# Kernel tuning notes

Measured on AMD Instinct MI355X. Metric: run time of the kernel, lower is better.

## Reference

```python
import jax, jax.numpy as jnp
import numpy as np

N_HEAD = 8
D_IN = 64
D_EMB = 128
B, S = 8, 2048
TEMP = D_EMB ** 0.5
EPS = 1e-6
NEG = -1e30


def setup_inputs() -> dict:
    key = jax.random.key(0)
    ks = jax.random.split(key, 10)
    Q = jax.random.normal(ks[0], (B, S, D_IN), jnp.float32)
    K = jax.random.normal(ks[1], (B, S, D_IN), jnp.float32)
    V = jax.random.normal(ks[2], (B, S, D_IN), jnp.float32)
    QMask = jax.random.randint(ks[3], (B, 1, 1, S), 0, 2).astype(jnp.float32)
    s_in = 1.0 / np.sqrt(D_IN)
    s_emb = 1.0 / np.sqrt(D_EMB)
    s_cat = 1.0 / np.sqrt(N_HEAD * D_EMB)
    W_in = jax.random.uniform(ks[4], (D_EMB, D_IN), jnp.float32, -s_in, s_in)
    W_mh = jax.random.uniform(ks[5], (N_HEAD * D_EMB, D_EMB), jnp.float32, -s_emb, s_emb)
    W_fc = jax.random.uniform(ks[6], (D_EMB, N_HEAD * D_EMB), jnp.float32, -s_cat, s_cat)
    ln_g = jnp.ones((D_EMB,), jnp.float32)
    ln_b = jnp.zeros((D_EMB,), jnp.float32)
    return {"Q": Q, "K": K, "V": V, "QMask": QMask,
            "W_in": W_in, "W_mh": W_mh, "W_fc": W_fc,
            "ln_g": ln_g, "ln_b": ln_b}


def reference(Q, K, V, QMask, W_in, W_mh, W_fc, ln_g, ln_b):
    b, ql = Q.shape[0], Q.shape[1]
    kl = K.shape[1]
    # shared input embedding
    Qe = jnp.einsum('bsi,ei->bse', Q, W_in)  # [B,Sq,D_EMB]
    Ke = jnp.einsum('bsi,ei->bse', K, W_in)
    Ve = jnp.einsum('bsi,ei->bse', V, W_in)
    residual = Qe
    # multi-head projection -> [B,S,H,D] -> [B,H,S,D]
    q = jnp.einsum('bse,fe->bsf', Qe, W_mh).reshape(b, ql, N_HEAD, D_EMB).transpose(0, 2, 1, 3)
    k = jnp.einsum('bse,fe->bsf', Ke, W_mh).reshape(b, kl, N_HEAD, D_EMB).transpose(0, 2, 1, 3)
    v = jnp.einsum('bse,fe->bsf', Ve, W_mh).reshape(b, kl, N_HEAD, D_EMB).transpose(0, 2, 1, 3)
    attn = jnp.einsum('bhqd,bhkd->bhqk', q / TEMP, k)
    attn = attn + (1.0 - QMask) * NEG
    attn = jax.nn.softmax(attn, axis=-1)
    out = jnp.einsum('bhqk,bhkd->bhqd', attn, v)  # [B,H,Sq,D]
    # faithful to original: view without transposing heads back
    out = out.reshape(b, ql, N_HEAD * D_EMB)
    out = jnp.einsum('bsf,ef->bse', out, W_fc) + residual
    mu = jnp.mean(out, axis=-1, keepdims=True)
    var = jnp.var(out, axis=-1, keepdims=True)
    out = (out - mu) / jnp.sqrt(var + EPS) * ln_g + ln_b
    return out
```

## Files before the change

### kernel.cpp

```cpp
#include <hip/hip_runtime.h>
#include <hip/hip_bf16.h>
#include <cstdint>

typedef __attribute__((ext_vector_type(8))) short short8;
typedef __attribute__((ext_vector_type(4))) float f32x4;
typedef __attribute__((ext_vector_type(16))) float f32x16;
typedef unsigned short u16;
typedef unsigned int u32;

__device__ __forceinline__ u16 f2bf(float f) {
    union { float f; u32 u; } v; v.f = f;
    u32 u = v.u;
    u = (u + 0x7fffu + ((u >> 16) & 1u)) >> 16;
    return (u16)u;
}

__device__ __forceinline__ float fexp2(float x) {
    float r;
    asm("v_exp_f32 %0, %1" : "=v"(r) : "v"(x));
    return r;
}

__device__ __forceinline__ u32 pk_bf16(float lo, float hi) {
    u32 r;
    asm("v_cvt_pk_bf16_f32 %0, %1, %2" : "=v"(r) : "v"(lo), "v"(hi));
    return r;
}

__device__ __forceinline__ void pl32swap(u32& a, u32& b) {
#if __has_builtin(__builtin_amdgcn_permlane32_swap)
    auto r = __builtin_amdgcn_permlane32_swap((int)a, (int)b, false, false);
    a = (u32)r[0]; b = (u32)r[1];
#else
    u32 ax = (u32)__shfl_xor((int)a, 32), bx = (u32)__shfl_xor((int)b, 32);
    bool hi = (threadIdx.x & 32) != 0;
    u32 na = hi ? bx : a;
    u32 nb = hi ? b : ax;
    a = na; b = nb;
#endif
}

__device__ __forceinline__ void gload_lds16(const u16* g, u16* l) {
    __builtin_amdgcn_global_load_lds((const __attribute__((address_space(1))) void*)g,
                                     (__attribute__((address_space(3))) void*)l, 16, 0, 0);
}

__device__ __forceinline__ short8 make_pa(float p0, float p1, float p2, float p3,
                                          float p4, float p5, float p6, float p7) {
    u32 a1 = pk_bf16(p0, p1), b1 = pk_bf16(p4, p5);
    u32 a2 = pk_bf16(p2, p3), b2 = pk_bf16(p6, p7);
    pl32swap(a1, b1); pl32swap(a2, b2);
    union { u32 w[4]; short8 s; } u;
    u.w[0] = a1; u.w[1] = a2; u.w[2] = b1; u.w[3] = b2;
    return u.s;
}

__global__ void prep_kernel(const float* __restrict__ W_in,
                            const float* __restrict__ W_mh,
                            const float* __restrict__ W_fc,
                            const float* __restrict__ qmask,
                            u16* __restrict__ wcomb, u16* __restrict__ wfc16,
                            u16* __restrict__ win16,
                            u16* __restrict__ pos, int* __restrict__ cnt) {
    if (blockIdx.x >= 800) {
        if (threadIdx.x >= 64) return;
        int b = blockIdx.x - 800, t = threadIdx.x;
        int base = b * 2048 + t * 32;
        int c = 0;
#pragma unroll
        for (int i = 0; i < 32; ++i) c += (qmask[base + i] != 0.0f) ? 1 : 0;
        int inc = c;
#pragma unroll
        for (int dd = 1; dd < 64; dd <<= 1) {
            int v = __shfl_up(inc, dd);
            if (t >= dd) inc += v;
        }
        int run = inc - c;
#pragma unroll
        for (int i = 0; i < 32; ++i) {
            bool mk = (qmask[base + i] != 0.0f);
            pos[base + i] = mk ? (u16)run : (u16)0xFFFF;
            run += mk ? 1 : 0;
        }
        if (t == 63) cnt[b] = inc;
        return;
    }
    int idx = blockIdx.x * 256 + threadIdx.x;
    if (idx < 1024 * 64) {
        int f = idx >> 6, i = idx & 63;
        float acc = 0.f;
        for (int e = 0; e < 128; ++e)
            acc += W_mh[f * 128 + e] * W_in[e * 64 + i];
        wcomb[idx] = f2bf(acc);
    }
    int idx2 = idx - 65536;
    if (idx2 >= 0 && idx2 < 128 * 1024)
        wfc16[idx2] = f2bf(W_fc[idx2]);
    int idx3 = idx - 65536 - 131072;
    if (idx3 >= 0 && idx3 < 128 * 64)
        win16[idx3] = f2bf(W_in[idx3]);
}

__global__ __launch_bounds__(256) void qkv_kernel(
    const float* __restrict__ K, const float* __restrict__ V,
    const u16* __restrict__ wcomb, const u16* __restrict__ pos,
    u16* __restrict__ kb, u16* __restrict__ vrow) {
    __shared__ __align__(16) u16 ot[64 * 264];
    int w = threadIdx.x >> 6, lane = threadIdx.x & 63;
    int g = lane >> 4, c15 = lane & 15;
    const float* X = blockIdx.z == 0 ? K : V;

    int Rrow = blockIdx.x * 64 + w * 16 + c15;
    short8 af[2];
#pragma unroll
    for (int c = 0; c < 2; ++c) {
        const float* p = X + (size_t)Rrow * 64 + 8 * g + 32 * c;
        float4 fa = *(const float4*)(p);
        float4 fb = *(const float4*)(p + 4);
        short8 a;
        a[0] = (short)f2bf(fa.x); a[1] = (short)f2bf(fa.y);
        a[2] = (short)f2bf(fa.z); a[3] = (short)f2bf(fa.w);
        a[4] = (short)f2bf(fb.x); a[5] = (short)f2bf(fb.y);
        a[6] = (short)f2bf(fb.z); a[7] = (short)f2bf(fb.w);
        af[c] = a;
    }
    int colbase = blockIdx.y * 256;
    f32x4 acc[16];
#pragma unroll
    for (int i = 0; i < 16; ++i) acc[i] = {0.f, 0.f, 0.f, 0.f};
#pragma unroll
    for (int cb = 0; cb < 16; ++cb) {
        int col = colbase + cb * 16 + c15;
#pragma unroll
        for (int c = 0; c < 2; ++c) {
            short8 bfr = *(const short8*)(wcomb + (size_t)col * 64 + 8 * g + 32 * c);
            acc[cb] = __builtin_amdgcn_mfma_f32_16x16x32_bf16(af[c], bfr, acc[cb], 0, 0, 0);
        }
    }
    int r0 = w * 16 + 4 * g;
#pragma unroll
    for (int cb = 0; cb < 16; ++cb)
#pragma unroll
        for (int r = 0; r < 4; ++r)
            ot[(r0 + r) * 264 + cb * 16 + c15] = f2bf(acc[cb][r]);
    __syncthreads();
    u16* dstbuf = blockIdx.z == 0 ? kb : vrow;
#pragma unroll
    for (int it = 0; it < 8; ++it) {
        int chunk = threadIdx.x + it * 256;
        int row = chunk >> 5, cc = chunk & 31;
        int R = blockIdx.x * 64 + row;
        u16 p = pos[R];
        if (p != 0xFFFF) {
            int b = R >> 11;
            int col0 = colbase + cc * 8;
            int h = col0 >> 7, d = col0 & 127;
            *(uint4*)(dstbuf + ((size_t)(b * 8 + h) * 2048 + p) * 128 + d) =
                *(const uint4*)(ot + row * 264 + cc * 8);
        }
    }
}

__global__ __launch_bounds__(256) void vtrans_kernel(
    const u16* __restrict__ vrow, const int* __restrict__ cnt,
    u16* __restrict__ vT) {
    int t = blockIdx.x, bh = blockIdx.y, b = bh >> 3;
    int L = cnt[b];
    if (t * 64 >= L) return;
    __shared__ __align__(16) u32 tl[128 * 32];
    const u16* src = vrow + ((size_t)bh * 2048 + t * 64) * 128;
#pragma unroll
    for (int task = 0; task < 2; ++task) {
        int id = threadIdx.x + task * 256;
        int i = id >> 4, c = id & 15;
        int r0 = 2 * i, r1 = 2 * i + 1;
        uint4 A = {0, 0, 0, 0}, Bv = {0, 0, 0, 0};
        if (t * 64 + r0 < L) A  = *(const uint4*)(src + (size_t)r0 * 128 + c * 8);
        if (t * 64 + r1 < L) Bv = *(const uint4*)(src + (size_t)r1 * 128 + c * 8);
        const u32* aw = (const u32*)&A;
        const u32* bw = (const u32*)&Bv;
#pragma unroll
        for (int j = 0; j < 4; ++j) {
            u32 lo  = (aw[j] & 0xFFFFu) | (bw[j] << 16);
            u32 hi2 = (aw[j] >> 16) | (bw[j] & 0xFFFF0000u);
            int d0 = 8 * c + 2 * j, d1 = d0 + 1;
            int h0 = ((d0 & 7) ^ ((d0 >> 3) & 7)) << 2;
            int h1 = ((d1 & 7) ^ ((d1 >> 3) & 7)) << 2;
            tl[d0 * 32 + (i ^ h0)] = lo;
            tl[d1 * 32 + (i ^ h1)] = hi2;
        }
    }
    __syncthreads();
    int d = threadIdx.x >> 1, half = threadIdx.x & 1;
    int hd = (d & 7) ^ ((d >> 3) & 7);
#pragma unroll
    for (int jc = 0; jc < 4; ++jc) {
        int chunk = (half * 4 + jc) ^ hd;
        int kcg = t * 8 + half * 4 + jc;
        *(uint4*)(vT + (((size_t)bh * 256 + kcg) * 128 + d) * 8) =
            *(const uint4*)(&tl[d * 32 + chunk * 4]);
    }
}

__global__ __launch_bounds__(512, 2) void attn_kernel(
    const float* __restrict__ Qin, const u16* __restrict__ wcomb,
    const u16* __restrict__ kbuf, const u16* __restrict__ vTc,
    const int* __restrict__ cnt,
    const u16* __restrict__ wfc16, const u16* __restrict__ win16,
    const float* __restrict__ ln_g, const float* __restrict__ ln_b,
    float* __restrict__ out) {
    __shared__ __align__(16) u16 smem[32768];
    __shared__ float2 pls[32][4];

    const int w = threadIdx.x >> 6, lane = threadIdx.x & 63;
    const int hi = lane >> 5, l31 = lane & 31;
    const int g = lane >> 4, c15 = lane & 15;
    const int bh = blockIdx.x, qt = blockIdx.y;
    const int b = bh >> 3, h = bh & 7;
    const int L = cnt[b];
    const int nt = (L + 63) >> 6;

    const u16* kbbh = kbuf + (size_t)bh * 2048 * 128;
    const u16* vTbh = vTc + (size_t)bh * 262144;

    u16* ktb0 = smem;
    u16* vtb0 = smem + 16384;

    auto stage = [&](int buf, int tt) {
#pragma unroll
        for (int c = 0; c < 2; ++c) {
            int rl = (c * 8 + w) * 4 + (lane >> 4);
            int ck = (lane & 15) ^ (rl & 7);
            gload_lds16(kbbh + ((size_t)(tt * 64 + rl)) * 128 + ck * 8,
                        ktb0 + buf * 8192 + (c * 8 + w) * 512);
            int ci = c * 512 + w * 64 + lane;
            gload_lds16(vTbh + ((size_t)tt * 1024 + ci) * 8,
                        vtb0 + buf * 8192 + (c * 512 + w * 64) * 8);
        }
    };

    stage(0, 0);

    const float invT2 = 0.12751743f;
    const int q0 = qt * 256 + w * 32;
    const float* qrow = Qin + ((size_t)b * 2048 + q0 + l31) * 64;
    short8 bq[4];
#pragma unroll
    for (int s = 0; s < 4; ++s) {
        const float* p = qrow + s * 16 + hi * 8;
        float4 fa = *(const float4*)(p);
        float4 fb = *(const float4*)(p + 4);
        short8 a;
        a[0] = (short)f2bf(fa.x); a[1] = (short)f2bf(fa.y);
        a[2] = (short)f2bf(fa.z); a[3] = (short)f2bf(fa.w);
        a[4] = (short)f2bf(fb.x); a[5] = (short)f2bf(fb.y);
        a[6] = (short)f2bf(fb.z); a[7] = (short)f2bf(fb.w);
        bq[s] = a;
    }
    short8 qf[8];
#pragma unroll
    for (int dblk = 0; dblk < 4; ++dblk) {
        f32x16 c2;
#pragma unroll
        for (int r = 0; r < 16; ++r) c2[r] = 0.f;
        const u16* wrow = wcomb + (size_t)(h * 128 + dblk * 32 + l31) * 64 + hi * 8;
#pragma unroll
        for (int s = 0; s < 4; ++s) {
            short8 wa = *(const short8*)(wrow + s * 16);
            c2 = __builtin_amdgcn_mfma_f32_32x32x16_bf16(wa, bq[s], c2, 0, 0, 0);
        }
        qf[2 * dblk] = make_pa(c2[0] * invT2, c2[1] * invT2, c2[2] * invT2, c2[3] * invT2,
                               c2[4] * invT2, c2[5] * invT2, c2[6] * invT2, c2[7] * invT2);
        qf[2 * dblk + 1] = make_pa(c2[8] * invT2, c2[9] * invT2, c2[10] * invT2, c2[11] * invT2,
                                   c2[12] * invT2, c2[13] * invT2, c2[14] * invT2, c2[15] * invT2);
    }

    f32x16 o[4];
#pragma unroll
    for (int i = 0; i < 4; ++i)
#pragma unroll
        for (int r = 0; r < 16; ++r) o[i][r] = 0.f;
    float m = -1e30f, lsum = 0.f;

    int cur = 0;
    __syncthreads();

    for (int t = 0; t < nt; ++t) {
        if (t + 1 < nt) stage(cur ^ 1, t + 1);
        const u16* ktb = ktb0 + cur * 8192;
        const u16* vtb = vtb0 + cur * 8192;

        f32x16 st0, st1;
#pragma unroll
        for (int r = 0; r < 16; ++r) { st0[r] = 0.f; st1[r] = 0.f; }
        int k0 = l31, k1 = 32 + l31;
#pragma unroll
        for (int ds = 0; ds < 8; ++ds) {
            int sw = ((ds * 2 + hi) ^ (l31 & 7)) << 3;
            short8 kf0 = *(const short8*)(ktb + (k0 << 7) + sw);
            short8 kf1 = *(const short8*)(ktb + (k1 << 7) + sw);
            st0 = __builtin_amdgcn_mfma_f32_32x32x16_bf16(kf0, qf[ds], st0, 0, 0, 0);
            st1 = __builtin_amdgcn_mfma_f32_32x32x16_bf16(kf1, qf[ds], st1, 0, 0, 0);
        }
        if (t == nt - 1) {
#pragma unroll
            for (int r = 0; r < 16; ++r) {
                int kl = (r & 3) + 8 * (r >> 2) + 4 * hi;
                st0[r] = (t * 64 + kl < L) ? st0[r] : -1e30f;
                st1[r] = (t * 64 + 32 + kl < L) ? st1[r] : -1e30f;
            }
        }
        float mx = st0[0];
#pragma unroll
        for (int r = 1; r < 16; ++r) mx = fmaxf(mx, st0[r]);
#pragma unroll
        for (int r = 0; r < 16; ++r) mx = fmaxf(mx, st1[r]);
        mx = fmaxf(mx, __shfl_xor(mx, 32));
        if (__any(mx - m > 11.0f)) {
            float mn = fmaxf(m, mx);
            float corr = fexp2(m - mn);
            m = mn;
            lsum *= corr;
#pragma unroll
            for (int r = 0; r < 16; ++r) {
                float cc = __shfl(corr, (r & 3) + 8 * (r >> 2) + 4 * hi);
                o[0][r] *= cc; o[1][r] *= cc; o[2][r] *= cc; o[3][r] *= cc;
            }
        }
        float p0a[16], p1a[16];
#pragma unroll
        for (int r = 0; r < 16; ++r) { p0a[r] = fexp2(st0[r] - m); p1a[r] = fexp2(st1[r] - m); }
        float s0 = 0.f, s1 = 0.f, s2 = 0.f, s3 = 0.f;
#pragma unroll
        for (int r = 0; r < 16; r += 4) {
            s0 += p0a[r]; s1 += p0a[r + 1]; s2 += p0a[r + 2]; s3 += p0a[r + 3];
            s0 += p1a[r]; s1 += p1a[r + 1]; s2 += p1a[r + 2]; s3 += p1a[r + 3];
        }
        float tot = (s0 + s1) + (s2 + s3);
        tot += __shfl_xor(tot, 32);
        lsum += tot;
        short8 pa0 = make_pa(p0a[0], p0a[1], p0a[2], p0a[3], p0a[4], p0a[5], p0a[6], p0a[7]);
        short8 pa1 = make_pa(p0a[8], p0a[9], p0a[10], p0a[11], p0a[12], p0a[13], p0a[14], p0a[15]);
        short8 pa2 = make_pa(p1a[0], p1a[1], p1a[2], p1a[3], p1a[4], p1a[5], p1a[6], p1a[7]);
        short8 pa3 = make_pa(p1a[8], p1a[9], p1a[10], p1a[11], p1a[12], p1a[13], p1a[14], p1a[15]);
#pragma unroll
        for (int dblk = 0; dblk < 4; ++dblk) {
#pragma unroll
            for (int ks = 0; ks < 4; ++ks) {
                short8 vf = *(const short8*)(vtb +
                    ((((ks * 2 + hi) << 7) + (dblk << 5) + l31) << 3));
                short8 pa = (ks == 0) ? pa0 : (ks == 1) ? pa1 : (ks == 2) ? pa2 : pa3;
                o[dblk] = __builtin_amdgcn_mfma_f32_32x32x16_bf16(pa, vf, o[dblk], 0, 0, 0);
            }
        }
        __syncthreads();
        cur ^= 1;
    }

    u16* epi = smem;
    float invl = 1.0f / lsum;
#pragma unroll
    for (int r = 0; r < 16; ++r) {
        int kl = (r & 3) + 8 * (r >> 2) + 4 * hi;
        float iv = __shfl(invl, kl);
        int row_local = w * 4 + (kl >> 3);
        int cb2 = (kl & 7) * 16 + (l31 >> 3);
#pragma unroll
        for (int dblk = 0; dblk < 4; ++dblk) {
            int cw = cb2 + dblk * 4;
            epi[(cw * 32 + row_local) * 8 + (l31 & 7)] = f2bf(o[dblk][r] * iv);
        }
    }
    __syncthreads();

    const int rg = w >> 2, cg = w & 3;
    const int srow0 = h * 256 + qt * 32;
    const int row16 = rg * 16 + c15;
    f32x4 acA[2], acB[2];
    acA[0] = {0.f, 0.f, 0.f, 0.f}; acA[1] = {0.f, 0.f, 0.f, 0.f};
    acB[0] = {0.f, 0.f, 0.f, 0.f}; acB[1] = {0.f, 0.f, 0.f, 0.f};
    {
        const float* p0 = Qin + ((size_t)b * 2048 + srow0 + row16) * 64;
        short8 af2[2];
#pragma unroll
        for (int c = 0; c < 2; ++c) {
            float4 fa = *(const float4*)(p0 + 8 * g + 32 * c);
            float4 fb = *(const float4*)(p0 + 8 * g + 32 * c + 4);
            short8 a;
            a[0] = (short)f2bf(fa.x); a[1] = (short)f2bf(fa.y);
            a[2] = (short)f2bf(fa.z); a[3] = (short)f2bf(fa.w);
            a[4] = (short)f2bf(fb.x); a[5] = (short)f2bf(fb.y);
            a[6] = (short)f2bf(fb.z); a[7] = (short)f2bf(fb.w);
            af2[c] = a;
        }
#pragma unroll
        for (int eb = 0; eb < 2; ++eb)
#pragma unroll
            for (int c = 0; c < 2; ++c) {
                short8 bfr = *(const short8*)(win16 +
                    (size_t)(cg * 32 + eb * 16 + c15) * 64 + 8 * g + 32 * c);
                acA[eb] = __builtin_amdgcn_mfma_f32_16x16x32_bf16(af2[c], bfr, acA[eb], 0, 0, 0);
            }
    }
#pragma unroll
    for (int kc2 = 0; kc2 < 16; ++kc2) {
        int kcE = 2 * kc2, kcO = 2 * kc2 + 1;
        short8 afE = *(const short8*)(epi + ((kcE * 4 + g) * 32 + row16) * 8);
        short8 afO = *(const short8*)(epi + ((kcO * 4 + g) * 32 + row16) * 8);
#pragma unroll
        for (int eb = 0; eb < 2; ++eb) {
            short8 bfE = *(const short8*)(wfc16 +
                (size_t)(cg * 32 + eb * 16 + c15) * 1024 + kcE * 32 + 8 * g);
            short8 bfO = *(const short8*)(wfc16 +
                (size_t)(cg * 32 + eb * 16 + c15) * 1024 + kcO * 32 + 8 * g);
            acA[eb] = __builtin_amdgcn_mfma_f32_16x16x32_bf16(afE, bfE, acA[eb], 0, 0, 0);
            acB[eb] = __builtin_amdgcn_mfma_f32_16x16x32_bf16(afO, bfO, acB[eb], 0, 0, 0);
        }
    }
    f32x4 acc2[2];
#pragma unroll
    for (int eb = 0; eb < 2; ++eb)
#pragma unroll
        for (int r = 0; r < 4; ++r)
            acc2[eb][r] = acA[eb][r] + acB[eb][r];
#pragma unroll
    for (int r = 0; r < 4; ++r) {
        float s = acc2[0][r] + acc2[1][r];
        float q2 = acc2[0][r] * acc2[0][r] + acc2[1][r] * acc2[1][r];
#pragma unroll
        for (int dd = 1; dd < 16; dd <<= 1) {
            s += __shfl_xor(s, dd);
            q2 += __shfl_xor(q2, dd);
        }
        if (c15 == 0) pls[rg * 16 + 4 * g + r][cg] = make_float2(s, q2);
    }
    __syncthreads();
    float gg0 = ln_g[cg * 32 + c15],      bb0 = ln_b[cg * 32 + c15];
    float gg1 = ln_g[cg * 32 + 16 + c15], bb1 = ln_b[cg * 32 + 16 + c15];
#pragma unroll
    for (int r = 0; r < 4; ++r) {
        int row = rg * 16 + 4 * g + r;
        float2 pa = pls[row][0], pb = pls[row][1], pc = pls[row][2], pd = pls[row][3];
        float mean = (pa.x + pb.x + pc.x + pd.x) * (1.0f / 128.0f);
        float var  = (pa.y + pb.y + pc.y + pd.y) * (1.0f / 128.0f) - mean * mean;
        float rstd = rsqrtf(var + 1e-6f);
        size_t ob = ((size_t)b * 2048 + srow0 + row) * 128;
        out[ob + cg * 32 + c15]      = (acc2[0][r] - mean) * rstd * gg0 + bb0;
        out[ob + cg * 32 + 16 + c15] = (acc2[1][r] - mean) * rstd * gg1 + bb1;
    }
}

extern "C" void kernel_launch(void* const* d_in, const int* in_sizes, int n_in,
                              void* d_out, int out_size, void* d_ws, size_t ws_size,
                              hipStream_t stream) {
    const float* Q     = (const float*)d_in[0];
    const float* K     = (const float*)d_in[1];
    const float* V     = (const float*)d_in[2];
    const float* QMask = (const float*)d_in[3];
    const float* W_in  = (const float*)d_in[4];
    const float* W_mh  = (const float*)d_in[5];
    const float* W_fc  = (const float*)d_in[6];
    const float* ln_g  = (const float*)d_in[7];
    const float* ln_b  = (const float*)d_in[8];
    float* out = (float*)d_out;

    char* ws = (char*)d_ws;
    u16*   wcomb = (u16*)(ws);
    u16*   wfc16 = (u16*)(ws + 131072);
    u16*   kb    = (u16*)(ws + 42336256);
    u16*   vT    = (u16*)(ws + 75890688);
    u16*   vrow  = (u16*)(ws + 109445120);
    u16*   pos   = (u16*)(ws + 142999552);
    int*   cnt   = (int*)(ws + 143032320);
    u16*   win16 = (u16*)(ws + 143036416);

    hipLaunchKernelGGL(prep_kernel, dim3(808), dim3(256), 0, stream,
                       W_in, W_mh, W_fc, QMask, wcomb, wfc16, win16, pos, cnt);
    hipLaunchKernelGGL(qkv_kernel, dim3(256, 4, 2), dim3(256), 0, stream,
                       K, V, wcomb, pos, kb, vrow);
    hipLaunchKernelGGL(vtrans_kernel, dim3(32, 64), dim3(256), 0, stream,
                       vrow, cnt, vT);
    hipLaunchKernelGGL(attn_kernel, dim3(64, 8), dim3(512), 0, stream,
                       Q, wcomb, kb, vT, cnt, wfc16, win16, ln_g, ln_b, out);
}
```

Baseline: 176.7 us.

## Fuse V projection into V-transpose kernel via inverse compaction index

V is no longer projected in qkv_kernel and written to a compacted row-major bf16 buffer. Instead vtrans_kernel gathers the unmasked V rows through a new inverse index built in prep_kernel, projects them with MFMA into shared memory, and transposes them directly into vT. This removes one global write and one global read of the intermediate V buffer. The attention epilogue's shared-memory layout also gains a padded stride of 264, which likely avoids LDS bank conflicts and slightly enlarges shared memory. The cost is uncoalesced gathered V row reads and projection work now sitting inside the transpose kernel.

```diff
diff --git a/kernel.cpp b/kernel.cpp
--- a/kernel.cpp
+++ b/kernel.cpp
@@ -61,7 +61,8 @@
                             const float* __restrict__ qmask,
                             u16* __restrict__ wcomb, u16* __restrict__ wfc16,
                             u16* __restrict__ win16,
-                            u16* __restrict__ pos, int* __restrict__ cnt) {
+                            u16* __restrict__ pos, u16* __restrict__ inv,
+                            int* __restrict__ cnt) {
     if (blockIdx.x >= 800) {
         if (threadIdx.x >= 64) return;
         int b = blockIdx.x - 800, t = threadIdx.x;
@@ -80,6 +81,7 @@
         for (int i = 0; i < 32; ++i) {
             bool mk = (qmask[base + i] != 0.0f);
             pos[base + i] = mk ? (u16)run : (u16)0xFFFF;
+            if (mk) inv[b * 2048 + run] = (u16)(t * 32 + i);
             run += mk ? 1 : 0;
         }
         if (t == 63) cnt[b] = inc;
@@ -102,19 +104,18 @@
 }
 
 __global__ __launch_bounds__(256) void qkv_kernel(
-    const float* __restrict__ K, const float* __restrict__ V,
+    const float* __restrict__ K,
     const u16* __restrict__ wcomb, const u16* __restrict__ pos,
-    u16* __restrict__ kb, u16* __restrict__ vrow) {
+    u16* __restrict__ kb) {
     __shared__ __align__(16) u16 ot[64 * 264];
     int w = threadIdx.x >> 6, lane = threadIdx.x & 63;
     int g = lane >> 4, c15 = lane & 15;
-    const float* X = blockIdx.z == 0 ? K : V;
 
     int Rrow = blockIdx.x * 64 + w * 16 + c15;
     short8 af[2];
 #pragma unroll
     for (int c = 0; c < 2; ++c) {
-        const float* p = X + (size_t)Rrow * 64 + 8 * g + 32 * c;
+        const float* p = K + (size_t)Rrow * 64 + 8 * g + 32 * c;
         float4 fa = *(const float4*)(p);
         float4 fb = *(const float4*)(p + 4);
         short8 a;
@@ -144,7 +145,6 @@
         for (int r = 0; r < 4; ++r)
             ot[(r0 + r) * 264 + cb * 16 + c15] = f2bf(acc[cb][r]);
     __syncthreads();
-    u16* dstbuf = blockIdx.z == 0 ? kb : vrow;
 #pragma unroll
     for (int it = 0; it < 8; ++it) {
         int chunk = threadIdx.x + it * 256;
@@ -155,28 +155,69 @@
             int b = R >> 11;
             int col0 = colbase + cc * 8;
             int h = col0 >> 7, d = col0 & 127;
-            *(uint4*)(dstbuf + ((size_t)(b * 8 + h) * 2048 + p) * 128 + d) =
+            *(uint4*)(kb + ((size_t)(b * 8 + h) * 2048 + p) * 128 + d) =
                 *(const uint4*)(ot + row * 264 + cc * 8);
         }
     }
 }
 
 __global__ __launch_bounds__(256) void vtrans_kernel(
-    const u16* __restrict__ vrow, const int* __restrict__ cnt,
+    const float* __restrict__ V, const u16* __restrict__ wcomb,
+    const u16* __restrict__ inv, const int* __restrict__ cnt,
     u16* __restrict__ vT) {
-    int t = blockIdx.x, bh = blockIdx.y, b = bh >> 3;
+    int t = blockIdx.x, bh = blockIdx.y, b = bh >> 3, h = bh & 7;
     int L = cnt[b];
     if (t * 64 >= L) return;
+    __shared__ __align__(16) u16 ot[64 * 136];
     __shared__ __align__(16) u32 tl[128 * 32];
-    const u16* src = vrow + ((size_t)bh * 2048 + t * 64) * 128;
+
+    int w = threadIdx.x >> 6, lane = threadIdx.x & 63;
+    int g = lane >> 4, c15 = lane & 15;
+
+    int lr = w * 16 + c15;
+    bool okr = (t * 64 + lr < L);
+    int src = okr ? (int)inv[b * 2048 + t * 64 + lr] : 0;
+    short8 af[2] = {};
+    if (okr) {
+        const float* p0 = V + ((size_t)b * 2048 + src) * 64;
+#pragma unroll
+        for (int c = 0; c < 2; ++c) {
+            float4 fa = *(const float4*)(p0 + 8 * g + 32 * c);
+            float4 fb = *(const float4*)(p0 + 8 * g + 32 * c + 4);
+            short8 a;
+            a[0] = (short)f2bf(fa.x); a[1] = (short)f2bf(fa.y);
+            a[2] = (short)f2bf(fa.z); a[3] = (short)f2bf(fa.w);
+            a[4] = (short)f2bf(fb.x); a[5] = (short)f2bf(fb.y);
+            a[6] = (short)f2bf(fb.z); a[7] = (short)f2bf(fb.w);
+            af[c] = a;
+        }
+    }
+    f32x4 acc[8];
+#pragma unroll
+    for (int i = 0; i < 8; ++i) acc[i] = {0.f, 0.f, 0.f, 0.f};
+#pragma unroll
+    for (int cb = 0; cb < 8; ++cb) {
+        int col = h * 128 + cb * 16 + c15;
+#pragma unroll
+        for (int c = 0; c < 2; ++c) {
+            short8 bfr = *(const short8*)(wcomb + (size_t)col * 64 + 8 * g + 32 * c);
+            acc[cb] = __builtin_amdgcn_mfma_f32_16x16x32_bf16(af[c], bfr, acc[cb], 0, 0, 0);
+        }
+    }
+    int rr0 = w * 16 + 4 * g;
+#pragma unroll
+    for (int cb = 0; cb < 8; ++cb)
+#pragma unroll
+        for (int r = 0; r < 4; ++r)
+            ot[(rr0 + r) * 136 + cb * 16 + c15] = f2bf(acc[cb][r]);
+    __syncthreads();
+
 #pragma unroll
     for (int task = 0; task < 2; ++task) {
         int id = threadIdx.x + task * 256;
         int i = id >> 4, c = id & 15;
-        int r0 = 2 * i, r1 = 2 * i + 1;
-        uint4 A = {0, 0, 0, 0}, Bv = {0, 0, 0, 0};
-        if (t * 64 + r0 < L) A  = *(const uint4*)(src + (size_t)r0 * 128 + c * 8);
-        if (t * 64 + r1 < L) Bv = *(const uint4*)(src + (size_t)r1 * 128 + c * 8);
+        uint4 A  = *(const uint4*)(ot + (2 * i) * 136 + c * 8);
+        uint4 Bv = *(const uint4*)(ot + (2 * i + 1) * 136 + c * 8);
         const u32* aw = (const u32*)&A;
         const u32* bw = (const u32*)&Bv;
 #pragma unroll
@@ -209,7 +250,7 @@
     const u16* __restrict__ wfc16, const u16* __restrict__ win16,
     const float* __restrict__ ln_g, const float* __restrict__ ln_b,
     float* __restrict__ out) {
-    __shared__ __align__(16) u16 smem[32768];
+    __shared__ __align__(16) u16 smem[33792];
     __shared__ float2 pls[32][4];
 
     const int w = threadIdx.x >> 6, lane = threadIdx.x & 63;
@@ -368,7 +409,7 @@
 #pragma unroll
         for (int dblk = 0; dblk < 4; ++dblk) {
             int cw = cb2 + dblk * 4;
-            epi[(cw * 32 + row_local) * 8 + (l31 & 7)] = f2bf(o[dblk][r] * iv);
+            epi[cw * 264 + row_local * 8 + (l31 & 7)] = f2bf(o[dblk][r] * iv);
         }
     }
     __syncthreads();
@@ -405,8 +446,8 @@
 #pragma unroll
     for (int kc2 = 0; kc2 < 16; ++kc2) {
         int kcE = 2 * kc2, kcO = 2 * kc2 + 1;
-        short8 afE = *(const short8*)(epi + ((kcE * 4 + g) * 32 + row16) * 8);
-        short8 afO = *(const short8*)(epi + ((kcO * 4 + g) * 32 + row16) * 8);
+        short8 afE = *(const short8*)(epi + (kcE * 4 + g) * 264 + row16 * 8);
+        short8 afO = *(const short8*)(epi + (kcO * 4 + g) * 264 + row16 * 8);
 #pragma unroll
         for (int eb = 0; eb < 2; ++eb) {
             short8 bfE = *(const short8*)(wfc16 +
@@ -469,17 +510,17 @@
     u16*   wfc16 = (u16*)(ws + 131072);
     u16*   kb    = (u16*)(ws + 42336256);
     u16*   vT    = (u16*)(ws + 75890688);
-    u16*   vrow  = (u16*)(ws + 109445120);
     u16*   pos   = (u16*)(ws + 142999552);
     int*   cnt   = (int*)(ws + 143032320);
     u16*   win16 = (u16*)(ws + 143036416);
+    u16*   inv   = (u16*)(ws + 143052800);
 
     hipLaunchKernelGGL(prep_kernel, dim3(808), dim3(256), 0, stream,
-                       W_in, W_mh, W_fc, QMask, wcomb, wfc16, win16, pos, cnt);
-    hipLaunchKernelGGL(qkv_kernel, dim3(256, 4, 2), dim3(256), 0, stream,
-                       K, V, wcomb, pos, kb, vrow);
+                       W_in, W_mh, W_fc, QMask, wcomb, wfc16, win16, pos, inv, cnt);
+    hipLaunchKernelGGL(qkv_kernel, dim3(256, 4), dim3(256), 0, stream,
+                       K, wcomb, pos, kb);
     hipLaunchKernelGGL(vtrans_kernel, dim3(32, 64), dim3(256), 0, stream,
-                       vrow, cnt, vT);
+                       V, wcomb, inv, cnt, vT);
     hipLaunchKernelGGL(attn_kernel, dim3(64, 8), dim3(512), 0, stream,
                        Q, wcomb, kb, vT, cnt, wfc16, win16, ln_g, ln_b, out);
 }
```

Measured after the change: 179.7 us. Within noise of the previous version (+1.7%).
